# Kernel tuning notes

Measured on AMD Instinct MI355X. Metric: run time of the kernel, lower is better.

Reference implementation:

```python
import jax, jax.numpy as jnp
import numpy as np

B, N, C, H, K = 1, 4096, 512, 8, 33
D = C // H
SCALE = D ** -0.5
EPS = 1e-5


def layernorm_nobias(x, g):
    m = jnp.mean(x, axis=-1, keepdims=True)
    v = jnp.mean(jnp.square(x - m), axis=-1, keepdims=True)
    return (x - m) * jax.lax.rsqrt(v + EPS) * g


def attn_layer(x, ln_g, wqkv, wproj, bproj, res_k):
    # x: [B, N1, C]
    Bq, Nq, Cq = x.shape
    h = layernorm_nobias(x, ln_g)
    qkv = (h @ wqkv.T).reshape(Bq, Nq, 3, H, D).transpose(2, 0, 3, 1, 4)  # [3,B,H,N1,D]
    q, k, v = qkv[0], qkv[1], qkv[2]
    scores = jnp.einsum('bhnd,bhmd->bhnm', q, k) * SCALE  # [B,H,N1,N1]
    a = jax.nn.softmax(scores, axis=-1)
    o = jnp.einsum('bhnm,bhmd->bhnd', a, v)
    o = o.transpose(0, 2, 1, 3).reshape(Bq, Nq, Cq)
    # depthwise 'talking-positions' residual conv over sequence dim of v
    res = jax.lax.conv_general_dilated(
        v, res_k, window_strides=(1, 1),
        padding=((K // 2, K // 2), (0, 0)),
        dimension_numbers=('NCHW', 'OIHW', 'NCHW'),
        feature_group_count=H)  # [B,H,N1,D]
    o = o + res.transpose(0, 2, 1, 3).reshape(Bq, Nq, Cq)
    return x + o @ wproj.T + bproj


def setup_inputs() -> dict:
    key = jax.random.key(0)
    ks = jax.random.split(key, 10)
    w = 0.02
    return {
        'x': jax.random.normal(ks[0], (B, N, C), jnp.float32),
        'cls_token': jax.random.normal(ks[1], (1, 1, C), jnp.float32) * 1e-6,
        'ln_g1': jnp.ones((C,), jnp.float32),
        'wqkv1': jax.random.normal(ks[2], (3 * C, C), jnp.float32) * w,
        'wproj1': jax.random.normal(ks[3], (C, C), jnp.float32) * w,
        'bproj1': jnp.zeros((C,), jnp.float32),
        'resk1': jax.random.normal(ks[4], (H, 1, K, 1), jnp.float32) * 0.05,
        'ln_g2': jnp.ones((C,), jnp.float32),
        'wqkv2': jax.random.normal(ks[5], (3 * C, C), jnp.float32) * w,
        'wproj2': jax.random.normal(ks[6], (C, C), jnp.float32) * w,
        'bproj2': jnp.zeros((C,), jnp.float32),
        'resk2': jax.random.normal(ks[7], (H, 1, K, 1), jnp.float32) * 0.05,
        'fc_g': jnp.ones((C,), jnp.float32),
    }


def reference(x, cls_token, ln_g1, wqkv1, wproj1, bproj1, resk1,
              ln_g2, wqkv2, wproj2, bproj2, resk2, fc_g):
    cls = jnp.broadcast_to(cls_token, (x.shape[0], 1, x.shape[2]))
    h = jnp.concatenate([cls, x], axis=1)  # [B, N+1, C]
    h = attn_layer(h, ln_g1, wqkv1, wproj1, bproj1, resk1)
    h = attn_layer(h, ln_g2, wqkv2, wproj2, bproj2, resk2)
    pooled = h[:, 0]  # cls token pooling, norm=Identity (fc_norm=True)
    return layernorm_nobias(pooled, fc_g)  # [B, C]
```

## Files before the change

kernel.cpp:

```cpp
#include <hip/hip_runtime.h>
#include <math.h>

#define NTOK 4097
#define CDIM 512
#define EPS_LN 1e-5f

typedef float f32x4 __attribute__((ext_vector_type(4)));
typedef __bf16 bf16x8 __attribute__((ext_vector_type(8)));

__device__ inline unsigned short f2bf(float f){
    union { float f; unsigned u; } c; c.f = f;
    unsigned u = c.u;
    unsigned r = (u + 0x7fffu + ((u >> 16) & 1u)) >> 16;
    return (unsigned short)r;
}
__device__ inline float bf2f(unsigned short b){
    union { unsigned u; float f; } c; c.u = ((unsigned)b) << 16;
    return c.f;
}
__device__ inline unsigned cvt_pk_bf16(float lo, float hi){
    unsigned r;
    asm("v_cvt_pk_bf16_f32 %0, %1, %2" : "=v"(r) : "v"(lo), "v"(hi));
    return r;
}

__global__ void concat_kernel(const float* __restrict__ x, const float* __restrict__ cls,
                              float* __restrict__ h0, int total){
    int idx = blockIdx.x * 256 + threadIdx.x;
    if (idx >= total) return;
    int n = idx >> 9;
    int c = idx & 511;
    h0[idx] = (n == 0) ? cls[c] : x[(size_t)(n - 1) * CDIM + c];
}

__global__ void cast_bf_kernel(const float* __restrict__ src, unsigned short* __restrict__ dst, int n){
    int i = (blockIdx.x * 256 + threadIdx.x) * 4;
    if (i >= n) return;
    float4 v = *(const float4*)(src + i);
    ushort4 o;
    o.x = f2bf(v.x); o.y = f2bf(v.y); o.z = f2bf(v.z); o.w = f2bf(v.w);
    *(ushort4*)(dst + i) = o;
}

__global__ __launch_bounds__(256) void ln_kernel(const float* __restrict__ in,
                                                 const float* __restrict__ g,
                                                 unsigned short* __restrict__ out){
    int n = blockIdx.x;
    const float* row = in + (size_t)n * CDIM;
    int t = threadIdx.x;
    float x0 = row[t], x1 = row[t + 256];
    float s = x0 + x1, q = x0 * x0 + x1 * x1;
    for (int o = 32; o > 0; o >>= 1) { s += __shfl_down(s, o); q += __shfl_down(q, o); }
    __shared__ float rs[4], rq[4], mv[2];
    int wid = t >> 6;
    if ((t & 63) == 0) { rs[wid] = s; rq[wid] = q; }
    __syncthreads();
    if (t == 0) {
        float S = rs[0] + rs[1] + rs[2] + rs[3];
        float Q = rq[0] + rq[1] + rq[2] + rq[3];
        float m = S / 512.0f;
        float v = Q / 512.0f - m * m;
        mv[0] = m; mv[1] = rsqrtf(v + EPS_LN);
    }
    __syncthreads();
    float m = mv[0], r = mv[1];
    unsigned short* orow = out + (size_t)n * CDIM;
    orow[t]       = f2bf((x0 - m) * r * g[t]);
    orow[t + 256] = f2bf((x1 - m) * r * g[t + 256]);
}

__global__ __launch_bounds__(256) void gemm_bf16(const unsigned short* __restrict__ A,
                                                 const unsigned short* __restrict__ B,
                                                 const float* __restrict__ resid,
                                                 const float* __restrict__ bias,
                                                 void* __restrict__ Cout, int M, int N, int obf){
    __shared__ unsigned short As[128][72];
    __shared__ unsigned short Bs[128][72];
    int t = threadIdx.x;
    int wave = t >> 6, lane = t & 63;
    int wr = wave >> 1, wc = wave & 1;
    int bm = blockIdx.x, bn = blockIdx.y;
    f32x4 acc[4][4] = {};
    int lrow = t >> 3;
    int lc8 = (t & 7) * 8;
    for (int k0 = 0; k0 < 512; k0 += 64) {
        __syncthreads();
        #pragma unroll
        for (int i = 0; i < 4; i++) {
            int row = lrow + i * 32;
            int ar = bm * 128 + row; if (ar > M - 1) ar = M - 1;
            int br = bn * 128 + row;
            *(uint4*)(&As[row][lc8]) = *(const uint4*)(A + (size_t)ar * 512 + k0 + lc8);
            *(uint4*)(&Bs[row][lc8]) = *(const uint4*)(B + (size_t)br * 512 + k0 + lc8);
        }
        __syncthreads();
        #pragma unroll
        for (int ks = 0; ks < 2; ks++) {
            bf16x8 af[4], bfr[4];
            #pragma unroll
            for (int mi = 0; mi < 4; mi++)
                af[mi] = *(const bf16x8*)(&As[wr * 64 + mi * 16 + (lane & 15)][ks * 32 + (lane >> 4) * 8]);
            #pragma unroll
            for (int ni = 0; ni < 4; ni++)
                bfr[ni] = *(const bf16x8*)(&Bs[wc * 64 + ni * 16 + (lane & 15)][ks * 32 + (lane >> 4) * 8]);
            #pragma unroll
            for (int mi = 0; mi < 4; mi++)
                #pragma unroll
                for (int ni = 0; ni < 4; ni++)
                    acc[mi][ni] = __builtin_amdgcn_mfma_f32_16x16x32_bf16(af[mi], bfr[ni], acc[mi][ni], 0, 0, 0);
        }
    }
    int n0 = bn * 128 + wc * 64;
    if (obf) {
        unsigned short* C = (unsigned short*)Cout;
        #pragma unroll
        for (int mi = 0; mi < 4; mi++)
            #pragma unroll
            for (int rg = 0; rg < 4; rg++) {
                int m = bm * 128 + wr * 64 + mi * 16 + (lane >> 4) * 4 + rg;
                if (m < M) {
                    unsigned short* crow = C + (size_t)m * N;
                    #pragma unroll
                    for (int ni = 0; ni < 4; ni++)
                        crow[n0 + ni * 16 + (lane & 15)] = f2bf(acc[mi][ni][rg]);
                }
            }
    } else {
        float* C = (float*)Cout;
        #pragma unroll
        for (int mi = 0; mi < 4; mi++)
            #pragma unroll
            for (int rg = 0; rg < 4; rg++) {
                int m = bm * 128 + wr * 64 + mi * 16 + (lane >> 4) * 4 + rg;
                if (m < M) {
                    float* crow = C + (size_t)m * N;
                    const float* rrow = resid ? resid + (size_t)m * N : nullptr;
                    #pragma unroll
                    for (int ni = 0; ni < 4; ni++) {
                        int n = n0 + ni * 16 + (lane & 15);
                        float v = acc[mi][ni][rg];
                        if (bias) v += bias[n];
                        if (rrow) v += rrow[n];
                        crow[n] = v;
                    }
                }
            }
    }
}

__global__ __launch_bounds__(256) void flash1_mfma(const unsigned short* __restrict__ qkvb,
                                                   float* __restrict__ opart, float* __restrict__ ml){
    __shared__ __align__(16) char smem[24576];
    unsigned short* Qs = (unsigned short*)smem;
    unsigned short* Ks = Qs + 4096;
    unsigned short* Vt = Ks + 4096;
    const int h = blockIdx.y, qb = blockIdx.x, sp = blockIdx.z;
    const int t = threadIdx.x;
    const int wave = t >> 6, lane = t & 63;
    const int g = lane >> 4, q = lane & 15;
    const int rr8 = t >> 3;
    const int dc8 = (t & 7) * 8;

    #pragma unroll
    for (int pp = 0; pp < 2; pp++) {
        int r = rr8 + pp * 32;
        int tok = qb * 64 + r;
        uint4 qv = make_uint4(0, 0, 0, 0);
        if (tok < NTOK) qv = *(const uint4*)(qkvb + (size_t)tok * 1536 + h * 64 + dc8);
        *(uint4*)((char*)Qs + ((r * 128 + dc8 * 2) ^ ((r & 7) << 4))) = qv;
    }

    f32x4 acco[4] = {};
    float m_run = -INFINITY, l_run = 0.f;
    const int ktbeg = sp * 33;
    const int ktend = sp ? 65 : 33;

    for (int kt = ktbeg; kt < ktend; kt++) {
        __syncthreads();
        #pragma unroll
        for (int pp = 0; pp < 2; pp++) {
            int r = rr8 + pp * 32;
            int tok = kt * 64 + r;
            uint4 kv8 = make_uint4(0, 0, 0, 0);
            uint4 vv8 = make_uint4(0, 0, 0, 0);
            if (tok < NTOK) {
                const unsigned short* base = qkvb + (size_t)tok * 1536 + 512 + h * 64 + dc8;
                kv8 = *(const uint4*)(base);
                vv8 = *(const uint4*)(base + 512);
            }
            *(uint4*)((char*)Ks + ((r * 128 + dc8 * 2) ^ ((r & 7) << 4))) = kv8;
            const unsigned short* vsrc = (const unsigned short*)&vv8;
            #pragma unroll
            for (int e = 0; e < 8; e++) {
                int d = dc8 + e;
                *(unsigned short*)((char*)Vt + ((d * 128 + r * 2) ^ ((d & 7) << 4))) = vsrc[e];
            }
        }
        __syncthreads();

        f32x4 accs[4] = {};
        #pragma unroll
        for (int ks = 0; ks < 2; ks++) {
            int qrow = wave * 16 + q;
            bf16x8 bq = *(const bf16x8*)((char*)Qs + ((qrow * 128 + ks * 64 + g * 16) ^ ((qrow & 7) << 4)));
            #pragma unroll
            for (int mt = 0; mt < 4; mt++) {
                int kr = mt * 16 + q;
                bf16x8 ak = *(const bf16x8*)((char*)Ks + ((kr * 128 + ks * 64 + g * 16) ^ ((kr & 7) << 4)));
                accs[mt] = __builtin_amdgcn_mfma_f32_16x16x32_bf16(ak, bq, accs[mt], 0, 0, 0);
            }
        }

        float pr[4][4];
        float tmax = -INFINITY;
        #pragma unroll
        for (int mt = 0; mt < 4; mt++)
            #pragma unroll
            for (int rg = 0; rg < 4; rg++) {
                float s = accs[mt][rg] * 0.125f;
                if (kt == 64 && (4096 + mt * 16 + g * 4 + rg) >= NTOK) s = -INFINITY;
                pr[mt][rg] = s;
                tmax = fmaxf(tmax, s);
            }
        tmax = fmaxf(tmax, __shfl_xor(tmax, 16));
        tmax = fmaxf(tmax, __shfl_xor(tmax, 32));
        float mn = fmaxf(m_run, tmax);
        float alpha = __expf(m_run - mn);
        float psum = 0.f;
        #pragma unroll
        for (int mt = 0; mt < 4; mt++)
            #pragma unroll
            for (int rg = 0; rg < 4; rg++) {
                float pv = __expf(pr[mt][rg] - mn);
                pr[mt][rg] = pv;
                psum += pv;
            }
        psum += __shfl_xor(psum, 16);
        psum += __shfl_xor(psum, 32);
        l_run = l_run * alpha + psum;
        m_run = mn;
        #pragma unroll
        for (int mt = 0; mt < 4; mt++)
            #pragma unroll
            for (int rg = 0; rg < 4; rg++)
                acco[mt][rg] *= alpha;

        unsigned pk[4][2];
        #pragma unroll
        for (int mt = 0; mt < 4; mt++) {
            pk[mt][0] = cvt_pk_bf16(pr[mt][0], pr[mt][1]);
            pk[mt][1] = cvt_pk_bf16(pr[mt][2], pr[mt][3]);
        }

        #pragma unroll
        for (int ks = 0; ks < 2; ks++) {
            union { unsigned w[4]; bf16x8 v; } bp;
            #pragma unroll
            for (int sh = 0; sh < 2; sh++)
                #pragma unroll
                for (int rp = 0; rp < 2; rp++) {
                    int src = ((g & 1) * 2 + sh) * 16 + q;
                    unsigned r0 = __shfl(pk[2 * ks + 0][rp], src);
                    unsigned r1 = __shfl(pk[2 * ks + 1][rp], src);
                    bp.w[sh * 2 + rp] = (g < 2) ? r0 : r1;
                }
            #pragma unroll
            for (int mt = 0; mt < 4; mt++) {
                int dr = mt * 16 + q;
                bf16x8 av = *(const bf16x8*)((char*)Vt + ((dr * 128 + ks * 64 + g * 16) ^ ((dr & 7) << 4)));
                acco[mt] = __builtin_amdgcn_mfma_f32_16x16x32_bf16(av, bp.v, acco[mt], 0, 0, 0);
            }
        }
    }

    __syncthreads();
    {
        int tok_ml = qb * 64 + wave * 16 + q;
        if (g == 0 && tok_ml < NTOK) {
            float* mlp = ml + ((size_t)(sp * 8 + h) * NTOK + tok_ml) * 2;
            mlp[0] = m_run;
            mlp[1] = l_run;
        }
    }
    float* ob = (float*)smem + wave * 16 * 68;
    #pragma unroll
    for (int mt = 0; mt < 4; mt++)
        #pragma unroll
        for (int rg = 0; rg < 4; rg++)
            ob[q * 68 + mt * 16 + g * 4 + rg] = acco[mt][rg];
    __syncthreads();
    {
        float* outp = opart + (size_t)sp * NTOK * 512;
        int ql = lane >> 2;
        int tok = qb * 64 + wave * 16 + ql;
        #pragma unroll
        for (int i = 0; i < 4; i++) {
            int c = (lane & 3) + i * 4;
            if (tok < NTOK)
                *(float4*)(outp + (size_t)tok * 512 + h * 64 + c * 4) = *(const float4*)(ob + ql * 68 + c * 4);
        }
    }
}

__global__ void flash_combine(const float* __restrict__ opart, const float* __restrict__ ml,
                              float* __restrict__ attn){
    int idx = blockIdx.x * 256 + threadIdx.x;
    if (idx >= NTOK * CDIM) return;
    int tok = idx >> 9, h = (idx & 511) >> 6;
    const float* ml0 = ml + ((size_t)h * NTOK + tok) * 2;
    const float* ml1 = ml + ((size_t)(8 + h) * NTOK + tok) * 2;
    float m0 = ml0[0], l0 = ml0[1];
    float m1 = ml1[0], l1 = ml1[1];
    float M = fmaxf(m0, m1);
    float a0 = __expf(m0 - M), a1 = __expf(m1 - M);
    float o0 = opart[idx];
    float o1 = opart[(size_t)NTOK * 512 + idx];
    attn[idx] = (o0 * a0 + o1 * a1) / (l0 * a0 + l1 * a1);
}

__global__ void convres_kernel(const unsigned short* __restrict__ qkvb, const float* __restrict__ rk,
                               const float* __restrict__ attn, unsigned short* __restrict__ attn_bf){
    int idx = blockIdx.x * 256 + threadIdx.x;
    if (idx >= NTOK * CDIM) return;
    int n = idx >> 9, hd = idx & 511, h = hd >> 6;
    float a = attn[idx];
    const float* kr = rk + h * 33;
    #pragma unroll
    for (int k = 0; k < 33; k++) {
        int mm = n + k - 16;
        if (mm >= 0 && mm < NTOK)
            a += bf2f(qkvb[(size_t)mm * 1536 + 1024 + hd]) * kr[k];
    }
    attn_bf[idx] = f2bf(a);
}

__global__ void qrow_kernel(const unsigned short* __restrict__ ln2b, const float* __restrict__ wqkv,
                            float* __restrict__ q2){
    int j = blockIdx.x;
    int lane = threadIdx.x;
    const float* w = wqkv + (size_t)j * 512;
    float s = 0.f;
    for (int k = lane; k < 512; k += 64) s += bf2f(ln2b[k]) * w[k];
    for (int o = 32; o > 0; o >>= 1) s += __shfl_down(s, o);
    if (lane == 0) q2[j] = s;
}

__global__ void srow_kernel(const float* __restrict__ q2, const unsigned short* __restrict__ kv2b,
                            float* __restrict__ srow){
    int mm = blockIdx.x * 256 + threadIdx.x;
    int h = blockIdx.y;
    if (mm >= NTOK) return;
    const float* q = q2 + h * 64;
    const unsigned short* k = kv2b + (size_t)mm * 1024 + h * 64;
    float s = 0.f;
    #pragma unroll
    for (int d = 0; d < 64; d++) s += q[d] * bf2f(k[d]);
    srow[(size_t)h * NTOK + mm] = s * 0.125f;
}

__global__ __launch_bounds__(256) void softmax_row(float* __restrict__ srow, float* __restrict__ Lout){
    int h = blockIdx.x, t = threadIdx.x;
    float* s = srow + (size_t)h * NTOK;
    __shared__ float red[4];
    float mx = -INFINITY;
    for (int i = t; i < NTOK; i += 256) mx = fmaxf(mx, s[i]);
    for (int o = 32; o > 0; o >>= 1) mx = fmaxf(mx, __shfl_xor(mx, o));
    if ((t & 63) == 0) red[t >> 6] = mx;
    __syncthreads();
    mx = fmaxf(fmaxf(red[0], red[1]), fmaxf(red[2], red[3]));
    __syncthreads();
    float sum = 0.f;
    for (int i = t; i < NTOK; i += 256) { float p = __expf(s[i] - mx); s[i] = p; sum += p; }
    for (int o = 32; o > 0; o >>= 1) sum += __shfl_xor(sum, o);
    if ((t & 63) == 0) red[t >> 6] = sum;
    __syncthreads();
    if (t == 0) Lout[h] = red[0] + red[1] + red[2] + red[3];
}

__global__ __launch_bounds__(256) void pv_row(const float* __restrict__ srow, const unsigned short* __restrict__ kv2b,
                                              const float* __restrict__ L, float* __restrict__ o2){
    int hd = blockIdx.x;
    int h = hd >> 6;
    int t = threadIdx.x;
    const float* p = srow + (size_t)h * NTOK;
    const unsigned short* v = kv2b + 512 + hd;
    float s = 0.f;
    for (int i = t; i < NTOK; i += 256) s += p[i] * bf2f(v[(size_t)i * 1024]);
    for (int o = 32; o > 0; o >>= 1) s += __shfl_down(s, o);
    __shared__ float red[4];
    if ((t & 63) == 0) red[t >> 6] = s;
    __syncthreads();
    if (t == 0) o2[hd] = (red[0] + red[1] + red[2] + red[3]) / L[h];
}

__global__ void conv0_kernel(const unsigned short* __restrict__ kv2b, const float* __restrict__ rk,
                             float* __restrict__ o2){
    int hd = threadIdx.x;
    int h = hd >> 6;
    float a = o2[hd];
    #pragma unroll
    for (int k = 16; k < 33; k++)
        a += bf2f(kv2b[(size_t)(k - 16) * 1024 + 512 + hd]) * rk[h * 33 + k];
    o2[hd] = a;
}

__global__ __launch_bounds__(512) void final_kernel(const float* __restrict__ h1, const float* __restrict__ o2,
                                                    const float* __restrict__ wproj, const float* __restrict__ bproj,
                                                    const float* __restrict__ fcg, float* __restrict__ out){
    __shared__ float ov[512];
    __shared__ float red_s[8], red_q[8], mv[2];
    int t = threadIdx.x;
    ov[t] = o2[t];
    __syncthreads();
    const float* w = wproj + (size_t)t * 512;
    float acc = h1[t] + bproj[t];
    for (int k = 0; k < 512; k++) acc += ov[k] * w[k];
    float s = acc, q = acc * acc;
    for (int o = 32; o > 0; o >>= 1) { s += __shfl_down(s, o); q += __shfl_down(q, o); }
    if ((t & 63) == 0) { red_s[t >> 6] = s; red_q[t >> 6] = q; }
    __syncthreads();
    if (t == 0) {
        float S = 0.f, Q = 0.f;
        for (int i = 0; i < 8; i++) { S += red_s[i]; Q += red_q[i]; }
        float m = S / 512.0f;
        float v = Q / 512.0f - m * m;
        mv[0] = m; mv[1] = rsqrtf(v + EPS_LN);
    }
    __syncthreads();
    out[t] = (acc - mv[0]) * mv[1] * fcg[t];
}

extern "C" void kernel_launch(void* const* d_in, const int* in_sizes, int n_in,
                              void* d_out, int out_size, void* d_ws, size_t ws_size,
                              hipStream_t stream){
    const float* x      = (const float*)d_in[0];
    const float* cls    = (const float*)d_in[1];
    const float* ln_g1  = (const float*)d_in[2];
    const float* wqkv1  = (const float*)d_in[3];
    const float* wproj1 = (const float*)d_in[4];
    const float* bproj1 = (const float*)d_in[5];
    const float* resk1  = (const float*)d_in[6];
    const float* ln_g2  = (const float*)d_in[7];
    const float* wqkv2  = (const float*)d_in[8];
    const float* wproj2 = (const float*)d_in[9];
    const float* bproj2 = (const float*)d_in[10];
    const float* resk2  = (const float*)d_in[11];
    const float* fc_g   = (const float*)d_in[12];
    float* out = (float*)d_out;
    float* ws  = (float*)d_ws;

    const size_t NC = (size_t)NTOK * 512;
    float* h0    = ws;
    unsigned short* qkvb = (unsigned short*)(h0 + NC);
    float* attn  = h0 + NC + (NC * 3) / 2;
    float* h1    = attn + NC;
    float* opart = attn;
    float* sm    = h1 + NC;
    float* q2    = sm;
    float* o2    = sm + 512;
    float* Lrow  = sm + 1024;
    float* srow  = sm + 2048;
    float* ml    = sm + 40960;
    unsigned short* bfbuf = (unsigned short*)(ml + 131104);
    unsigned short* wq1b  = bfbuf + NC;
    unsigned short* wp1b  = wq1b + 1536 * 512;
    unsigned short* wkv2b = wp1b + 512 * 512;
    unsigned short* kv2b  = qkvb;

    cast_bf_kernel<<<768, 256, 0, stream>>>(wqkv1, wq1b, 1536 * 512);
    cast_bf_kernel<<<256, 256, 0, stream>>>(wproj1, wp1b, 512 * 512);
    cast_bf_kernel<<<512, 256, 0, stream>>>(wqkv2 + (size_t)512 * 512, wkv2b, 1024 * 512);

    concat_kernel<<<8194, 256, 0, stream>>>(x, cls, h0, NTOK * CDIM);
    ln_kernel<<<NTOK, 256, 0, stream>>>(h0, ln_g1, bfbuf);
    gemm_bf16<<<dim3(33, 12), 256, 0, stream>>>(bfbuf, wq1b, nullptr, nullptr, qkvb, NTOK, 1536, 1);
    flash1_mfma<<<dim3(65, 8, 2), 256, 0, stream>>>(qkvb, opart, ml);
    flash_combine<<<8194, 256, 0, stream>>>(opart, ml, attn);
    convres_kernel<<<8194, 256, 0, stream>>>(qkvb, resk1, attn, bfbuf);
    gemm_bf16<<<dim3(33, 4), 256, 0, stream>>>(bfbuf, wp1b, h0, bproj1, h1, NTOK, 512, 0);

    ln_kernel<<<NTOK, 256, 0, stream>>>(h1, ln_g2, bfbuf);
    gemm_bf16<<<dim3(33, 8), 256, 0, stream>>>(bfbuf, wkv2b, nullptr, nullptr, kv2b, NTOK, 1024, 1);
    qrow_kernel<<<512, 64, 0, stream>>>(bfbuf, wqkv2, q2);
    srow_kernel<<<dim3(17, 8), 256, 0, stream>>>(q2, kv2b, srow);
    softmax_row<<<8, 256, 0, stream>>>(srow, Lrow);
    pv_row<<<512, 256, 0, stream>>>(srow, kv2b, Lrow, o2);
    conv0_kernel<<<1, 512, 0, stream>>>(kv2b, resk2, o2);
    final_kernel<<<1, 512, 0, stream>>>(h1, o2, wproj2, bproj2, fc_g, out);
}
```

Baseline: 440.9 us.

## Fuse flash combine into convres, reswizzle V tile, parallelize final projection

```diff
diff --git a/kernel.cpp b/kernel.cpp
--- a/kernel.cpp
+++ b/kernel.cpp
@@ -193,7 +193,7 @@
             #pragma unroll
             for (int e = 0; e < 8; e++) {
                 int d = dc8 + e;
-                *(unsigned short*)((char*)Vt + ((d * 128 + r * 2) ^ ((d & 7) << 4))) = vsrc[e];
+                *(unsigned short*)((char*)Vt + ((d * 128 + r * 2) ^ (((d & 7) ^ ((d >> 3) & 7)) << 4))) = vsrc[e];
             }
         }
         __syncthreads();
@@ -267,7 +267,7 @@
             #pragma unroll
             for (int mt = 0; mt < 4; mt++) {
                 int dr = mt * 16 + q;
-                bf16x8 av = *(const bf16x8*)((char*)Vt + ((dr * 128 + ks * 64 + g * 16) ^ ((dr & 7) << 4)));
+                bf16x8 av = *(const bf16x8*)((char*)Vt + ((dr * 128 + ks * 64 + g * 16) ^ (((dr & 7) ^ ((dr >> 3) & 7)) << 4)));
                 acco[mt] = __builtin_amdgcn_mfma_f32_16x16x32_bf16(av, bp.v, acco[mt], 0, 0, 0);
             }
         }
@@ -302,28 +302,21 @@
     }
 }
 
-__global__ void flash_combine(const float* __restrict__ opart, const float* __restrict__ ml,
-                              float* __restrict__ attn){
+__global__ void convres_kernel(const unsigned short* __restrict__ qkvb, const float* __restrict__ rk,
+                               const float* __restrict__ opart, const float* __restrict__ ml,
+                               unsigned short* __restrict__ attn_bf){
     int idx = blockIdx.x * 256 + threadIdx.x;
     if (idx >= NTOK * CDIM) return;
-    int tok = idx >> 9, h = (idx & 511) >> 6;
-    const float* ml0 = ml + ((size_t)h * NTOK + tok) * 2;
-    const float* ml1 = ml + ((size_t)(8 + h) * NTOK + tok) * 2;
+    int n = idx >> 9, hd = idx & 511, h = hd >> 6;
+    const float* ml0 = ml + ((size_t)h * NTOK + n) * 2;
+    const float* ml1 = ml + ((size_t)(8 + h) * NTOK + n) * 2;
     float m0 = ml0[0], l0 = ml0[1];
     float m1 = ml1[0], l1 = ml1[1];
     float M = fmaxf(m0, m1);
     float a0 = __expf(m0 - M), a1 = __expf(m1 - M);
     float o0 = opart[idx];
     float o1 = opart[(size_t)NTOK * 512 + idx];
-    attn[idx] = (o0 * a0 + o1 * a1) / (l0 * a0 + l1 * a1);
-}
-
-__global__ void convres_kernel(const unsigned short* __restrict__ qkvb, const float* __restrict__ rk,
-                               const float* __restrict__ attn, unsigned short* __restrict__ attn_bf){
-    int idx = blockIdx.x * 256 + threadIdx.x;
-    if (idx >= NTOK * CDIM) return;
-    int n = idx >> 9, hd = idx & 511, h = hd >> 6;
-    float a = attn[idx];
+    float a = (o0 * a0 + o1 * a1) / (l0 * a0 + l1 * a1);
     const float* kr = rk + h * 33;
     #pragma unroll
     for (int k = 0; k < 33; k++) {
@@ -404,17 +397,23 @@
     o2[hd] = a;
 }
 
-__global__ __launch_bounds__(512) void final_kernel(const float* __restrict__ h1, const float* __restrict__ o2,
-                                                    const float* __restrict__ wproj, const float* __restrict__ bproj,
-                                                    const float* __restrict__ fcg, float* __restrict__ out){
-    __shared__ float ov[512];
+__global__ void proj_row(const float* __restrict__ h1, const float* __restrict__ o2,
+                         const float* __restrict__ wproj, const float* __restrict__ bproj,
+                         float* __restrict__ pvec){
+    int j = blockIdx.x;
+    int lane = threadIdx.x;
+    const float* w = wproj + (size_t)j * 512;
+    float s = 0.f;
+    for (int k = lane; k < 512; k += 64) s += o2[k] * w[k];
+    for (int o = 32; o > 0; o >>= 1) s += __shfl_down(s, o);
+    if (lane == 0) pvec[j] = h1[j] + bproj[j] + s;
+}
+
+__global__ __launch_bounds__(512) void ln_final(const float* __restrict__ pvec,
+                                                const float* __restrict__ fcg, float* __restrict__ out){
     __shared__ float red_s[8], red_q[8], mv[2];
     int t = threadIdx.x;
-    ov[t] = o2[t];
-    __syncthreads();
-    const float* w = wproj + (size_t)t * 512;
-    float acc = h1[t] + bproj[t];
-    for (int k = 0; k < 512; k++) acc += ov[k] * w[k];
+    float acc = pvec[t];
     float s = acc, q = acc * acc;
     for (int o = 32; o > 0; o >>= 1) { s += __shfl_down(s, o); q += __shfl_down(q, o); }
     if ((t & 63) == 0) { red_s[t >> 6] = s; red_q[t >> 6] = q; }
@@ -452,13 +451,13 @@
     const size_t NC = (size_t)NTOK * 512;
     float* h0    = ws;
     unsigned short* qkvb = (unsigned short*)(h0 + NC);
-    float* attn  = h0 + NC + (NC * 3) / 2;
-    float* h1    = attn + NC;
-    float* opart = attn;
+    float* opart = h0 + NC + (NC * 3) / 2;
+    float* h1    = opart + NC;
     float* sm    = h1 + NC;
     float* q2    = sm;
     float* o2    = sm + 512;
     float* Lrow  = sm + 1024;
+    float* pvec  = sm + 1536;
     float* srow  = sm + 2048;
     float* ml    = sm + 40960;
     unsigned short* bfbuf = (unsigned short*)(ml + 131104);
@@ -475,8 +474,7 @@
     ln_kernel<<<NTOK, 256, 0, stream>>>(h0, ln_g1, bfbuf);
     gemm_bf16<<<dim3(33, 12), 256, 0, stream>>>(bfbuf, wq1b, nullptr, nullptr, qkvb, NTOK, 1536, 1);
     flash1_mfma<<<dim3(65, 8, 2), 256, 0, stream>>>(qkvb, opart, ml);
-    flash_combine<<<8194, 256, 0, stream>>>(opart, ml, attn);
-    convres_kernel<<<8194, 256, 0, stream>>>(qkvb, resk1, attn, bfbuf);
+    convres_kernel<<<8194, 256, 0, stream>>>(qkvb, resk1, opart, ml, bfbuf);
     gemm_bf16<<<dim3(33, 4), 256, 0, stream>>>(bfbuf, wp1b, h0, bproj1, h1, NTOK, 512, 0);
 
     ln_kernel<<<NTOK, 256, 0, stream>>>(h1, ln_g2, bfbuf);
@@ -486,5 +484,6 @@
     softmax_row<<<8, 256, 0, stream>>>(srow, Lrow);
     pv_row<<<512, 256, 0, stream>>>(srow, kv2b, Lrow, o2);
     conv0_kernel<<<1, 512, 0, stream>>>(kv2b, resk2, o2);
-    final_kernel<<<1, 512, 0, stream>>>(h1, o2, wproj2, bproj2, fc_g, out);
-}
+    proj_row<<<512, 64, 0, stream>>>(h1, o2, wproj2, bproj2, pvec);
+    ln_final<<<1, 512, 0, stream>>>(pvec, fc_g, out);
+}
```

Result: faster. 380.6 us (-13.7%).
